# Optimization experiments

Measured on AMD Instinct MI355X. Metric: run time of the kernel, lower is better.

The kernel has to match this reference:

```python
import jax, jax.numpy as jnp
import numpy as np

HIDDEN = 1024
VOCAB = 50257
MAXLEN = 64


def setup_inputs() -> dict:
    key = jax.random.key(0)
    ks = jax.random.split(key, 16)
    s = 0.02
    return {
        "token": jax.random.randint(ks[0], (1,), 0, VOCAB, dtype=jnp.int64),
        "hidden": jax.random.normal(ks[1], (1, 1, HIDDEN), dtype=jnp.float32),
        "encoder_outputs": jax.random.normal(ks[2], (MAXLEN, HIDDEN), dtype=jnp.float32),
        "emb": jax.random.normal(ks[3], (VOCAB, HIDDEN), dtype=jnp.float32) * s,
        "attn_W": jax.random.normal(ks[4], (MAXLEN, 2 * HIDDEN), dtype=jnp.float32) * s,
        "attn_b": jnp.zeros((MAXLEN,), dtype=jnp.float32),
        "comb_W": jax.random.normal(ks[5], (HIDDEN, 2 * HIDDEN), dtype=jnp.float32) * s,
        "comb_b": jnp.zeros((HIDDEN,), dtype=jnp.float32),
        "W_ih": jax.random.normal(ks[6], (3 * HIDDEN, HIDDEN), dtype=jnp.float32) * s,
        "W_hh": jax.random.normal(ks[7], (3 * HIDDEN, HIDDEN), dtype=jnp.float32) * s,
        "b_ih": jnp.zeros((3 * HIDDEN,), dtype=jnp.float32),
        "b_hh": jnp.zeros((3 * HIDDEN,), dtype=jnp.float32),
        "out_W": jax.random.normal(ks[8], (VOCAB, HIDDEN), dtype=jnp.float32) * s,
        "out_b": jnp.zeros((VOCAB,), dtype=jnp.float32),
    }


def reference(token, hidden, encoder_outputs, emb, attn_W, attn_b,
              comb_W, comb_b, W_ih, W_hh, b_ih, b_hh, out_W, out_b):
    # embedded: [1, H] (dropout is identity in eval mode)
    embedded = emb[token].reshape(1, -1)
    h0 = hidden[0]  # [1, H]
    # attention over the encoder window: [1, MAXLEN]
    scores = jnp.concatenate([embedded, h0], axis=1) @ attn_W.T + attn_b
    attn_weights = jax.nn.softmax(scores, axis=1)
    # context: [1, H]
    attn_applied = attn_weights @ encoder_outputs
    # combine + relu: [1, H]
    x = jnp.concatenate([embedded, attn_applied], axis=1) @ comb_W.T + comb_b
    x = jax.nn.relu(x)
    # single GRU step (PyTorch gate math)
    gi = x @ W_ih.T + b_ih    # [1, 3H]
    gh = h0 @ W_hh.T + b_hh   # [1, 3H]
    i_r, i_z, i_n = jnp.split(gi, 3, axis=1)
    h_r, h_z, h_n = jnp.split(gh, 3, axis=1)
    r = jax.nn.sigmoid(i_r + h_r)
    z = jax.nn.sigmoid(i_z + h_z)
    n = jnp.tanh(i_n + r * h_n)
    h_new = (1.0 - z) * n + z * h0  # [1, H]
    logits = h_new @ out_W.T + out_b  # [1, VOCAB]
    return logits, h_new[None, :, :], attn_weights
```

## Files before the change

kernel.cpp:

```cpp
#include <hip/hip_runtime.h>
#include <math.h>

#define HIDDEN 1024
#define VOCAB  50257
#define MAXLEN 64

__device__ __forceinline__ float wave_reduce_sum(float v) {
    #pragma unroll
    for (int off = 32; off > 0; off >>= 1)
        v += __shfl_down(v, off, 64);
    return v;
}

__global__ void k_scores(const int* __restrict__ token,
                         const float* __restrict__ emb,
                         const float* __restrict__ hidden,
                         const float* __restrict__ attn_W,
                         const float* __restrict__ attn_b,
                         float* __restrict__ ws_scores) {
    const int m = blockIdx.x;
    const int t = threadIdx.x;
    const float* erow = emb + (size_t)token[0] * HIDDEN;
    const float4* Wrow = (const float4*)(attn_W + (size_t)m * 2 * HIDDEN);
    float acc = 0.f;
    #pragma unroll
    for (int it = 0; it < 2; ++it) {
        int i = t + it * 256;
        float4 w4 = Wrow[i];
        int k = i * 4;
        const float* src = (k < HIDDEN) ? (erow + k) : (hidden + k - HIDDEN);
        float4 c4 = *(const float4*)src;
        acc += w4.x * c4.x + w4.y * c4.y + w4.z * c4.z + w4.w * c4.w;
    }
    __shared__ float part[4];
    acc = wave_reduce_sum(acc);
    const int wid = t >> 6, lane = t & 63;
    if (lane == 0) part[wid] = acc;
    __syncthreads();
    if (t == 0)
        ws_scores[m] = part[0] + part[1] + part[2] + part[3] + attn_b[m];
}

__global__ void k_smctx(const float* __restrict__ ws_scores,
                        const float* __restrict__ enc,
                        float* __restrict__ ws_ctx,
                        float* __restrict__ out_attn) {
    __shared__ float wsm[MAXLEN];
    const int t = threadIdx.x;
    const int wid = t >> 6, lane = t & 63;
    if (wid == 0) {
        float s = ws_scores[lane];
        float mx = s;
        #pragma unroll
        for (int off = 32; off > 0; off >>= 1) mx = fmaxf(mx, __shfl_xor(mx, off, 64));
        float e = expf(s - mx);
        float sum = e;
        #pragma unroll
        for (int off = 32; off > 0; off >>= 1) sum += __shfl_xor(sum, off, 64);
        float wv = e / sum;
        wsm[lane] = wv;
        if (blockIdx.x == 0) out_attn[lane] = wv;
    }
    __syncthreads();
    const int h = blockIdx.x * 256 + t;
    float acc = 0.f;
    #pragma unroll 8
    for (int m = 0; m < MAXLEN; ++m)
        acc += wsm[m] * enc[(size_t)m * HIDDEN + h];
    ws_ctx[h] = acc;
}

__global__ void k_combine(const int* __restrict__ token,
                          const float* __restrict__ emb,
                          const float* __restrict__ ws_ctx,
                          const float* __restrict__ comb_W,
                          const float* __restrict__ comb_b,
                          float* __restrict__ ws_x) {
    const int wid = threadIdx.x >> 6, lane = threadIdx.x & 63;
    const int j = blockIdx.x * 4 + wid;
    const float* erow = emb + (size_t)token[0] * HIDDEN;
    const float4* Wrow = (const float4*)(comb_W + (size_t)j * 2 * HIDDEN);
    float acc = 0.f;
    #pragma unroll
    for (int it = 0; it < 8; ++it) {
        int i = lane + it * 64;
        float4 w4 = Wrow[i];
        int k = i * 4;
        const float* src = (k < HIDDEN) ? (erow + k) : (ws_ctx + k - HIDDEN);
        float4 c4 = *(const float4*)src;
        acc += w4.x * c4.x + w4.y * c4.y + w4.z * c4.z + w4.w * c4.w;
    }
    acc = wave_reduce_sum(acc);
    if (lane == 0) ws_x[j] = fmaxf(acc + comb_b[j], 0.f);
}

__global__ __launch_bounds__(384) void k_gru(
    const float* __restrict__ ws_x,
    const float* __restrict__ hidden,
    const float* __restrict__ W_ih,
    const float* __restrict__ W_hh,
    const float* __restrict__ b_ih,
    const float* __restrict__ b_hh,
    float* __restrict__ ws_h,
    float* __restrict__ out_h)
{
    __shared__ float dval[6];
    const int j = blockIdx.x;
    const int q = threadIdx.x >> 6, lane = threadIdx.x & 63;
    const float* row = (q < 3)
        ? (W_ih + (size_t)(j + q * HIDDEN) * HIDDEN)
        : (W_hh + (size_t)(j + (q - 3) * HIDDEN) * HIDDEN);
    const float* vec = (q < 3) ? ws_x : hidden;
    const float4* W4 = (const float4*)row;
    const float4* v4 = (const float4*)vec;
    float acc = 0.f;
    #pragma unroll
    for (int it = 0; it < 4; ++it) {
        int i = lane + it * 64;
        float4 a = W4[i];
        float4 b = v4[i];
        acc += a.x * b.x + a.y * b.y + a.z * b.z + a.w * b.w;
    }
    acc = wave_reduce_sum(acc);
    if (lane == 0) dval[q] = acc;
    __syncthreads();
    if (threadIdx.x == 0) {
        float i_r = dval[0] + b_ih[j];
        float i_z = dval[1] + b_ih[j + HIDDEN];
        float i_n = dval[2] + b_ih[j + 2 * HIDDEN];
        float h_r = dval[3] + b_hh[j];
        float h_z = dval[4] + b_hh[j + HIDDEN];
        float h_n = dval[5] + b_hh[j + 2 * HIDDEN];
        float r = 1.f / (1.f + expf(-(i_r + h_r)));
        float z = 1.f / (1.f + expf(-(i_z + h_z)));
        float n = tanhf(i_n + r * h_n);
        float h0v = hidden[j];
        float hn = (1.f - z) * n + z * h0v;
        ws_h[j] = hn;
        out_h[j] = hn;
    }
}

__global__ __launch_bounds__(256) void k_logits(
    const float* __restrict__ ws_h,
    const float* __restrict__ out_W,
    const float* __restrict__ out_b,
    float* __restrict__ out_logits)
{
    const int t = threadIdx.x;
    const int wid = t >> 6, lane = t & 63;
    const float4* h4 = (const float4*)ws_h;
    const float4 hv0 = h4[lane];
    const float4 hv1 = h4[lane + 64];
    const float4 hv2 = h4[lane + 128];
    const float4 hv3 = h4[lane + 192];

    const int base = blockIdx.x * 16 + wid * 4;
    const float4* W[4];
    #pragma unroll
    for (int r = 0; r < 4; ++r) {
        int v = base + r;
        if (v > VOCAB - 1) v = VOCAB - 1;
        W[r] = (const float4*)(out_W + (size_t)v * HIDDEN);
    }

    float acc[4];
    #pragma unroll
    for (int r = 0; r < 4; ++r) {
        float4 a0 = W[r][lane];
        float4 a1 = W[r][lane + 64];
        float4 a2 = W[r][lane + 128];
        float4 a3 = W[r][lane + 192];
        float s;
        s  = a0.x * hv0.x + a0.y * hv0.y + a0.z * hv0.z + a0.w * hv0.w;
        s += a1.x * hv1.x + a1.y * hv1.y + a1.z * hv1.z + a1.w * hv1.w;
        s += a2.x * hv2.x + a2.y * hv2.y + a2.z * hv2.z + a2.w * hv2.w;
        s += a3.x * hv3.x + a3.y * hv3.y + a3.z * hv3.z + a3.w * hv3.w;
        acc[r] = s;
    }
    #pragma unroll
    for (int r = 0; r < 4; ++r)
        acc[r] = wave_reduce_sum(acc[r]);
    if (lane == 0) {
        #pragma unroll
        for (int r = 0; r < 4; ++r) {
            const int v = base + r;
            if (v < VOCAB) out_logits[v] = acc[r] + out_b[v];
        }
    }
}

extern "C" void kernel_launch(void* const* d_in, const int* in_sizes, int n_in,
                              void* d_out, int out_size, void* d_ws, size_t ws_size,
                              hipStream_t stream) {
    const int*   token  = (const int*)d_in[0];
    const float* hidden = (const float*)d_in[1];
    const float* enc    = (const float*)d_in[2];
    const float* emb    = (const float*)d_in[3];
    const float* attn_W = (const float*)d_in[4];
    const float* attn_b = (const float*)d_in[5];
    const float* comb_W = (const float*)d_in[6];
    const float* comb_b = (const float*)d_in[7];
    const float* W_ih   = (const float*)d_in[8];
    const float* W_hh   = (const float*)d_in[9];
    const float* b_ih   = (const float*)d_in[10];
    const float* b_hh   = (const float*)d_in[11];
    const float* out_W  = (const float*)d_in[12];
    const float* out_b  = (const float*)d_in[13];

    float* out = (float*)d_out;
    float* out_logits = out;
    float* out_h      = out + VOCAB;
    float* out_attn   = out + VOCAB + HIDDEN;

    float* ws = (float*)d_ws;
    float* ws_scores = ws;
    float* ws_ctx    = ws + 64;
    float* ws_x      = ws + 1088;
    float* ws_h      = ws + 2112;

    k_scores<<<MAXLEN, 256, 0, stream>>>(token, emb, hidden, attn_W, attn_b, ws_scores);
    k_smctx<<<HIDDEN / 256, 256, 0, stream>>>(ws_scores, enc, ws_ctx, out_attn);
    k_combine<<<HIDDEN / 4, 256, 0, stream>>>(token, emb, ws_ctx, comb_W, comb_b, ws_x);
    k_gru<<<HIDDEN, 384, 0, stream>>>(ws_x, hidden, W_ih, W_hh, b_ih, b_hh, ws_h, out_h);
    k_logits<<<(VOCAB + 15) / 16, 256, 0, stream>>>(ws_h, out_W, out_b, out_logits);
}
```

Before: 53.91 us.

## Fuse scores, softmax and context into one kernel using atomics; grid-stride logits

```diff
diff --git a/kernel.cpp b/kernel.cpp
--- a/kernel.cpp
+++ b/kernel.cpp
@@ -12,14 +12,20 @@
     return v;
 }
 
-__global__ void k_scores(const int* __restrict__ token,
-                         const float* __restrict__ emb,
-                         const float* __restrict__ hidden,
-                         const float* __restrict__ attn_W,
-                         const float* __restrict__ attn_b,
-                         float* __restrict__ ws_scores) {
+__global__ __launch_bounds__(256) void k_score_ctx(
+    const int* __restrict__ token,
+    const float* __restrict__ emb,
+    const float* __restrict__ hidden,
+    const float* __restrict__ attn_W,
+    const float* __restrict__ attn_b,
+    const float* __restrict__ enc,
+    float* __restrict__ ws_ctxnum,
+    float* __restrict__ ws_den,
+    float* __restrict__ ws_e)
+{
     const int m = blockIdx.x;
     const int t = threadIdx.x;
+    const int wid = t >> 6, lane = t & 63;
     const float* erow = emb + (size_t)token[0] * HIDDEN;
     const float4* Wrow = (const float4*)(attn_W + (size_t)m * 2 * HIDDEN);
     float acc = 0.f;
@@ -33,63 +39,61 @@
         acc += w4.x * c4.x + w4.y * c4.y + w4.z * c4.z + w4.w * c4.w;
     }
     __shared__ float part[4];
+    __shared__ float e_sh;
     acc = wave_reduce_sum(acc);
-    const int wid = t >> 6, lane = t & 63;
     if (lane == 0) part[wid] = acc;
     __syncthreads();
-    if (t == 0)
-        ws_scores[m] = part[0] + part[1] + part[2] + part[3] + attn_b[m];
-}
-
-__global__ void k_smctx(const float* __restrict__ ws_scores,
-                        const float* __restrict__ enc,
-                        float* __restrict__ ws_ctx,
-                        float* __restrict__ out_attn) {
-    __shared__ float wsm[MAXLEN];
-    const int t = threadIdx.x;
-    const int wid = t >> 6, lane = t & 63;
-    if (wid == 0) {
-        float s = ws_scores[lane];
-        float mx = s;
-        #pragma unroll
-        for (int off = 32; off > 0; off >>= 1) mx = fmaxf(mx, __shfl_xor(mx, off, 64));
-        float e = expf(s - mx);
-        float sum = e;
-        #pragma unroll
-        for (int off = 32; off > 0; off >>= 1) sum += __shfl_xor(sum, off, 64);
-        float wv = e / sum;
-        wsm[lane] = wv;
-        if (blockIdx.x == 0) out_attn[lane] = wv;
+    if (t == 0) {
+        float e = expf(part[0] + part[1] + part[2] + part[3] + attn_b[m]);
+        ws_e[m] = e;
+        e_sh = e;
+        atomicAdd(ws_den, e);
     }
     __syncthreads();
-    const int h = blockIdx.x * 256 + t;
-    float acc = 0.f;
-    #pragma unroll 8
-    for (int m = 0; m < MAXLEN; ++m)
-        acc += wsm[m] * enc[(size_t)m * HIDDEN + h];
-    ws_ctx[h] = acc;
-}
-
-__global__ void k_combine(const int* __restrict__ token,
-                          const float* __restrict__ emb,
-                          const float* __restrict__ ws_ctx,
-                          const float* __restrict__ comb_W,
-                          const float* __restrict__ comb_b,
-                          float* __restrict__ ws_x) {
+    const float e = e_sh;
+    const int h = t * 4;
+    const float4 ev = *(const float4*)(enc + (size_t)m * HIDDEN + h);
+    atomicAdd(&ws_ctxnum[h + 0], e * ev.x);
+    atomicAdd(&ws_ctxnum[h + 1], e * ev.y);
+    atomicAdd(&ws_ctxnum[h + 2], e * ev.z);
+    atomicAdd(&ws_ctxnum[h + 3], e * ev.w);
+}
+
+__global__ __launch_bounds__(256) void k_combine(
+    const int* __restrict__ token,
+    const float* __restrict__ emb,
+    const float* __restrict__ ws_ctxnum,
+    const float* __restrict__ ws_den,
+    const float* __restrict__ ws_e,
+    const float* __restrict__ comb_W,
+    const float* __restrict__ comb_b,
+    float* __restrict__ ws_x,
+    float* __restrict__ out_attn)
+{
     const int wid = threadIdx.x >> 6, lane = threadIdx.x & 63;
     const int j = blockIdx.x * 4 + wid;
-    const float* erow = emb + (size_t)token[0] * HIDDEN;
-    const float4* Wrow = (const float4*)(comb_W + (size_t)j * 2 * HIDDEN);
-    float acc = 0.f;
-    #pragma unroll
-    for (int it = 0; it < 8; ++it) {
+    const float inv_den = 1.0f / ws_den[0];
+    if (blockIdx.x == 0 && wid == 0)
+        out_attn[lane] = ws_e[lane] * inv_den;
+    const float4* e4 = (const float4*)(emb + (size_t)token[0] * HIDDEN);
+    const float4* c4 = (const float4*)ws_ctxnum;
+    const float4* Wr = (const float4*)(comb_W + (size_t)j * 2 * HIDDEN);
+    float acc_e = 0.f, acc_c = 0.f;
+    #pragma unroll
+    for (int it = 0; it < 4; ++it) {
         int i = lane + it * 64;
-        float4 w4 = Wrow[i];
-        int k = i * 4;
-        const float* src = (k < HIDDEN) ? (erow + k) : (ws_ctx + k - HIDDEN);
-        float4 c4 = *(const float4*)src;
-        acc += w4.x * c4.x + w4.y * c4.y + w4.z * c4.z + w4.w * c4.w;
-    }
+        float4 a = Wr[i];
+        float4 c = e4[i];
+        acc_e += a.x * c.x + a.y * c.y + a.z * c.z + a.w * c.w;
+    }
+    #pragma unroll
+    for (int it = 0; it < 4; ++it) {
+        int i = lane + it * 64;
+        float4 a = Wr[i + 256];
+        float4 c = c4[i];
+        acc_c += a.x * c.x + a.y * c.y + a.z * c.z + a.w * c.w;
+    }
+    float acc = acc_e + acc_c * inv_den;
     acc = wave_reduce_sum(acc);
     if (lane == 0) ws_x[j] = fmaxf(acc + comb_b[j], 0.f);
 }
@@ -155,37 +159,33 @@
     const float4 hv2 = h4[lane + 128];
     const float4 hv3 = h4[lane + 192];
 
-    const int base = blockIdx.x * 16 + wid * 4;
-    const float4* W[4];
-    #pragma unroll
-    for (int r = 0; r < 4; ++r) {
-        int v = base + r;
-        if (v > VOCAB - 1) v = VOCAB - 1;
-        W[r] = (const float4*)(out_W + (size_t)v * HIDDEN);
-    }
-
-    float acc[4];
-    #pragma unroll
-    for (int r = 0; r < 4; ++r) {
-        float4 a0 = W[r][lane];
-        float4 a1 = W[r][lane + 64];
-        float4 a2 = W[r][lane + 128];
-        float4 a3 = W[r][lane + 192];
-        float s;
-        s  = a0.x * hv0.x + a0.y * hv0.y + a0.z * hv0.z + a0.w * hv0.w;
-        s += a1.x * hv1.x + a1.y * hv1.y + a1.z * hv1.z + a1.w * hv1.w;
-        s += a2.x * hv2.x + a2.y * hv2.y + a2.z * hv2.z + a2.w * hv2.w;
-        s += a3.x * hv3.x + a3.y * hv3.y + a3.z * hv3.z + a3.w * hv3.w;
-        acc[r] = s;
-    }
-    #pragma unroll
-    for (int r = 0; r < 4; ++r)
-        acc[r] = wave_reduce_sum(acc[r]);
-    if (lane == 0) {
+    for (int base = blockIdx.x * 16 + wid * 4; base < VOCAB; base += gridDim.x * 16) {
+        float acc[4];
         #pragma unroll
         for (int r = 0; r < 4; ++r) {
-            const int v = base + r;
-            if (v < VOCAB) out_logits[v] = acc[r] + out_b[v];
+            int v = base + r;
+            if (v > VOCAB - 1) v = VOCAB - 1;
+            const float4* W = (const float4*)(out_W + (size_t)v * HIDDEN);
+            float4 a0 = W[lane];
+            float4 a1 = W[lane + 64];
+            float4 a2 = W[lane + 128];
+            float4 a3 = W[lane + 192];
+            float s;
+            s  = a0.x * hv0.x + a0.y * hv0.y + a0.z * hv0.z + a0.w * hv0.w;
+            s += a1.x * hv1.x + a1.y * hv1.y + a1.z * hv1.z + a1.w * hv1.w;
+            s += a2.x * hv2.x + a2.y * hv2.y + a2.z * hv2.z + a2.w * hv2.w;
+            s += a3.x * hv3.x + a3.y * hv3.y + a3.z * hv3.z + a3.w * hv3.w;
+            acc[r] = s;
+        }
+        #pragma unroll
+        for (int r = 0; r < 4; ++r)
+            acc[r] = wave_reduce_sum(acc[r]);
+        if (lane == 0) {
+            #pragma unroll
+            for (int r = 0; r < 4; ++r) {
+                const int v = base + r;
+                if (v < VOCAB) out_logits[v] = acc[r] + out_b[v];
+            }
         }
     }
 }
@@ -214,14 +214,17 @@
     float* out_attn   = out + VOCAB + HIDDEN;
 
     float* ws = (float*)d_ws;
-    float* ws_scores = ws;
-    float* ws_ctx    = ws + 64;
-    float* ws_x      = ws + 1088;
-    float* ws_h      = ws + 2112;
-
-    k_scores<<<MAXLEN, 256, 0, stream>>>(token, emb, hidden, attn_W, attn_b, ws_scores);
-    k_smctx<<<HIDDEN / 256, 256, 0, stream>>>(ws_scores, enc, ws_ctx, out_attn);
-    k_combine<<<HIDDEN / 4, 256, 0, stream>>>(token, emb, ws_ctx, comb_W, comb_b, ws_x);
+    float* ws_ctxnum = ws;
+    float* ws_den    = ws + 1024;
+    float* ws_e      = ws + 1056;
+    float* ws_x      = ws + 1152;
+    float* ws_h      = ws + 2176;
+
+    hipMemsetAsync(ws, 0, (1024 + 32) * sizeof(float), stream);
+    k_score_ctx<<<MAXLEN, 256, 0, stream>>>(token, emb, hidden, attn_W, attn_b,
+                                            enc, ws_ctxnum, ws_den, ws_e);
+    k_combine<<<HIDDEN / 4, 256, 0, stream>>>(token, emb, ws_ctxnum, ws_den, ws_e,
+                                              comb_W, comb_b, ws_x, out_attn);
     k_gru<<<HIDDEN, 384, 0, stream>>>(ws_x, hidden, W_ih, W_hh, b_ih, b_hh, ws_h, out_h);
-    k_logits<<<(VOCAB + 15) / 16, 256, 0, stream>>>(ws_h, out_W, out_b, out_logits);
-}
+    k_logits<<<1024, 256, 0, stream>>>(ws_h, out_W, out_b, out_logits);
+}
```

New measurement: 59.22 us. +9.9%, slower.
